# Optimization experiments

Measured on AMD Instinct MI355X. Metric: run time of the kernel, lower is better.

The kernel has to match this reference:

```python
import jax, jax.numpy as jnp
import numpy as np
from jax.ops import segment_sum

N_NODES = 100000
N_EDGES = 3200000
N_GRAPHS = 64


def gcn_conv(x, W, b, src, dst, n_nodes):
    # Linear transform first (PyG GCNConv applies lin before propagate)
    h = x @ W  # [N, out]
    # Add self loops
    loop = jnp.arange(n_nodes, dtype=src.dtype)
    s = jnp.concatenate([src, loop])
    d = jnp.concatenate([dst, loop])
    # Symmetric normalization deg^-1/2 (deg counts incoming edges incl. self loop)
    deg = segment_sum(jnp.ones_like(d, dtype=h.dtype), d, num_segments=n_nodes)
    dinv = jnp.where(deg > 0, jax.lax.rsqrt(deg), 0.0)
    norm = dinv[s] * dinv[d]  # [E+N]
    # Gather messages from source, scale, scatter-add to target
    msg = h[s] * norm[:, None]
    out = segment_sum(msg, d, num_segments=n_nodes)
    return out + b


def setup_inputs() -> dict:
    key = jax.random.key(0)
    ks = jax.random.split(key, 6)
    x = jax.random.normal(ks[0], (N_NODES, 128), dtype=jnp.float32)
    edge_index = jax.random.randint(ks[1], (2, N_EDGES), 0, N_NODES, dtype=jnp.int64)
    batch = jnp.sort(jax.random.randint(ks[2], (N_NODES,), 0, N_GRAPHS, dtype=jnp.int64))
    W1 = jax.random.normal(ks[3], (128, 256), dtype=jnp.float32) * (1.0 / np.sqrt(128))
    b1 = jnp.zeros((256,), dtype=jnp.float32)
    W2 = jax.random.normal(ks[4], (256, 128), dtype=jnp.float32) * (1.0 / np.sqrt(256))
    b2 = jnp.zeros((128,), dtype=jnp.float32)
    return {"x": x, "edge_index": edge_index, "batch": batch,
            "W1": W1, "b1": b1, "W2": W2, "b2": b2, "num_graphs": N_GRAPHS}


def reference(x, edge_index, batch, W1, b1, W2, b2, num_graphs):
    n_nodes = x.shape[0]
    src, dst = edge_index[0], edge_index[1]
    # dropout(p=0.6, training=False) is identity at inference
    h = jax.nn.relu(gcn_conv(x, W1, b1, src, dst, n_nodes))
    h = gcn_conv(h, W2, b2, src, dst, n_nodes)
    # global_mean_pool by graph id
    sums = segment_sum(h, batch, num_segments=num_graphs)
    counts = segment_sum(jnp.ones((n_nodes,), dtype=h.dtype), batch, num_segments=num_graphs)
    return sums / jnp.maximum(counts, 1.0)[:, None]
```

## Files before the change

### kernel.cpp

```cpp
#include <hip/hip_runtime.h>
#include <hip/hip_bf16.h>
#include <stdint.h>

#define N_NODES 100000
#define N_EDGES 3200000
#define N_GRAPHS 64
#define BSH 8
#define NB 391
#define G_SC 512
#define EPB 6250

typedef unsigned int u32;
typedef unsigned short u16;
typedef __attribute__((ext_vector_type(8))) short bf16x8;
typedef __attribute__((ext_vector_type(4))) float f32x4;

__device__ __forceinline__ float bf_lo(u32 u){ return __uint_as_float(u << 16); }
__device__ __forceinline__ float bf_hi(u32 u){ return __uint_as_float(u & 0xffff0000u); }
__device__ __forceinline__ u16 f2bf(float f){
    union { __hip_bfloat16 h; u16 u; } c; c.h = __float2bfloat16(f); return c.u;
}
__device__ __forceinline__ u32 pack2(float a, float b){
    return (u32)f2bf(a) | ((u32)f2bf(b) << 16);
}

__global__ __launch_bounds__(512) void k_hist(const int* __restrict__ dst,
                                              int* __restrict__ hist){
    __shared__ int h[NB];
    int tid = threadIdx.x, g = blockIdx.x;
    for (int i = tid; i < NB; i += 512) h[i] = 0;
    __syncthreads();
    const int2* d2 = reinterpret_cast<const int2*>(dst + g * EPB);
    for (int i = tid; i < EPB / 2; i += 512){
        int2 d = d2[i];
        atomicAdd(&h[d.x >> BSH], 1);
        atomicAdd(&h[d.y >> BSH], 1);
    }
    __syncthreads();
    for (int i = tid; i < NB; i += 512) hist[i * G_SC + g] = h[i];
}

__global__ __launch_bounds__(512) void k_colscan(const int* __restrict__ hist,
                                                 int* __restrict__ cursors,
                                                 int* __restrict__ btot){
    __shared__ int sm[512];
    int b = blockIdx.x, tid = threadIdx.x;
    int v = hist[b * G_SC + tid];
    sm[tid] = v; __syncthreads();
    for (int off = 1; off < 512; off <<= 1){
        int t = (tid >= off) ? sm[tid - off] : 0;
        __syncthreads(); sm[tid] += t; __syncthreads();
    }
    cursors[b * G_SC + tid] = sm[tid] - v;
    if (tid == 511) btot[b] = sm[511];
}

__global__ __launch_bounds__(512) void k_bscan(const int* __restrict__ btot,
                                               int* __restrict__ bbase){
    __shared__ int sm[512];
    int tid = threadIdx.x;
    int v = (tid < NB) ? btot[tid] : 0;
    sm[tid] = v; __syncthreads();
    for (int off = 1; off < 512; off <<= 1){
        int t = (tid >= off) ? sm[tid - off] : 0;
        __syncthreads(); sm[tid] += t; __syncthreads();
    }
    if (tid < NB) bbase[tid] = sm[tid] - v;
    if (tid == 0) bbase[NB] = N_EDGES;
}

__global__ __launch_bounds__(512) void k_scatter(const int* __restrict__ src,
                                                 const int* __restrict__ dst,
                                                 const int* __restrict__ cursors,
                                                 const int* __restrict__ bbase,
                                                 u32* __restrict__ pairs){
    __shared__ int cur[NB];
    int g = blockIdx.x, tid = threadIdx.x;
    for (int i = tid; i < NB; i += 512) cur[i] = cursors[i * G_SC + g] + bbase[i];
    __syncthreads();
    const int2* s2 = reinterpret_cast<const int2*>(src + g * EPB);
    const int2* d2 = reinterpret_cast<const int2*>(dst + g * EPB);
    for (int i = tid; i < EPB / 2; i += 512){
        int2 s = s2[i]; int2 d = d2[i];
        int p0 = atomicAdd(&cur[d.x >> BSH], 1);
        pairs[p0] = (u32)s.x | ((u32)(d.x & 255) << 24);
        int p1 = atomicAdd(&cur[d.y >> BSH], 1);
        pairs[p1] = (u32)s.y | ((u32)(d.y & 255) << 24);
    }
}

__global__ __launch_bounds__(512) void k_fine(const u32* __restrict__ pairs,
                                              const int* __restrict__ bbase,
                                              int* __restrict__ offsets,
                                              float* __restrict__ dinv,
                                              int* __restrict__ csr_src){
    __shared__ int ldeg[256];
    __shared__ int ssc[256];
    __shared__ int lcur[256];
    int b = blockIdx.x, tid = threadIdx.x;
    int node0 = b << BSH;
    if (tid < 256) ldeg[tid] = 0;
    __syncthreads();
    int e0 = bbase[b], e1 = bbase[b + 1];
    for (int e = e0 + tid; e < e1; e += 512)
        atomicAdd(&ldeg[pairs[e] >> 24], 1);
    __syncthreads();
    int myDeg = (tid < 256) ? ldeg[tid] : 0;
    if (tid < 256) ssc[tid] = myDeg;
    __syncthreads();
    for (int off = 1; off < 256; off <<= 1){
        int t = 0;
        if (tid >= off && tid < 256) t = ssc[tid - off];
        __syncthreads();
        if (tid < 256) ssc[tid] += t;
        __syncthreads();
    }
    if (tid < 256){
        int excl = ssc[tid] - myDeg;
        int n = node0 + tid;
        if (n <= N_NODES) offsets[n] = e0 + excl;
        if (n < N_NODES)  dinv[n] = rsqrtf((float)myDeg + 1.0f);
        lcur[tid] = e0 + excl;
    }
    __syncthreads();
    for (int e = e0 + tid; e < e1; e += 512){
        u32 p = pairs[e];
        int pos = atomicAdd(&lcur[p >> 24], 1);
        csr_src[pos] = (int)(p & 0xFFFFFFu);
    }
}

__global__ void k_cvt_x(const float* __restrict__ x, const float* __restrict__ dinv,
                        u32* __restrict__ xb){
    int i = blockIdx.x * blockDim.x + threadIdx.x;
    if (i < N_NODES * 32){
        float w = dinv[i >> 5];
        float4 f = reinterpret_cast<const float4*>(x)[i];
        uint2 p = make_uint2(pack2(f.x * w, f.y * w), pack2(f.z * w, f.w * w));
        reinterpret_cast<uint2*>(xb)[i] = p;
    }
}

__global__ void k_cvt_w(const float* __restrict__ W1, const float* __restrict__ W2,
                        u16* __restrict__ w1t, u16* __restrict__ w2t){
    int i = blockIdx.x * blockDim.x + threadIdx.x;
    if (i < 128 * 256){
        int n = i / 128, k = i % 128;
        w1t[i] = f2bf(W1[k * 256 + n]);
    } else {
        int j = i - 128 * 256;
        int n = j / 256, k = j % 256;
        w2t[j] = f2bf(W2[k * 128 + n]);
    }
}

template<bool OUT_BF16>
__global__ __launch_bounds__(256) void k_agg(const u32* __restrict__ X,
                      const int* __restrict__ offs, const int* __restrict__ csr_src,
                      const float* __restrict__ dinv, void* __restrict__ out){
    int lane = threadIdx.x & 63;
    int v = blockIdx.x * 4 + (threadIdx.x >> 6);
    u32 u = X[v * 64 + lane];
    float a0 = bf_lo(u), a1 = bf_hi(u);
    int e1 = offs[v + 1];
    for (int e = offs[v]; e < e1; e += 64){
        int idx = e + lane;
        int sv = (idx < e1) ? csr_src[idx] : 0;
        int cnt = min(64, e1 - e);
        int j = 0;
        for (; j + 8 <= cnt; j += 8){
            int s0 = __shfl(sv, j),   s1 = __shfl(sv, j+1), s2 = __shfl(sv, j+2), s3 = __shfl(sv, j+3);
            int s4 = __shfl(sv, j+4), s5 = __shfl(sv, j+5), s6 = __shfl(sv, j+6), s7 = __shfl(sv, j+7);
            u32 u0 = X[s0*64 + lane], u1 = X[s1*64 + lane], u2 = X[s2*64 + lane], u3 = X[s3*64 + lane];
            u32 u4 = X[s4*64 + lane], u5 = X[s5*64 + lane], u6 = X[s6*64 + lane], u7 = X[s7*64 + lane];
            a0 += (bf_lo(u0) + bf_lo(u1)) + (bf_lo(u2) + bf_lo(u3))
                + (bf_lo(u4) + bf_lo(u5)) + (bf_lo(u6) + bf_lo(u7));
            a1 += (bf_hi(u0) + bf_hi(u1)) + (bf_hi(u2) + bf_hi(u3))
                + (bf_hi(u4) + bf_hi(u5)) + (bf_hi(u6) + bf_hi(u7));
        }
        for (; j < cnt; j++){
            int s = __shfl(sv, j);
            u32 uu = X[s*64 + lane];
            a0 += bf_lo(uu); a1 += bf_hi(uu);
        }
    }
    float w = dinv[v];
    a0 *= w; a1 *= w;
    if (OUT_BF16){
        ((u32*)out)[v*64 + lane] = pack2(a0, a1);
    } else {
        ((float2*)out)[v*64 + lane] = make_float2(a0, a1);
    }
}

template<int BK, int BN, bool RELU, bool BIAS, bool SCALE>
__global__ __launch_bounds__(256) void k_gemm(const u16* __restrict__ A, const u16* __restrict__ BT,
                        const float* __restrict__ bias, const float* __restrict__ rowscale,
                        u16* __restrict__ C, int M){
    __shared__ char As[64 * BK * 2];
    const int tid = threadIdx.x;
    const int rowbytes = BK * 2;
    const int units = 8 * BK;
    for (int it = tid; it < units; it += 256){
        int flat = it * 16;
        int r = flat / rowbytes, cb = flat % rowbytes;
        int grow = blockIdx.x * 64 + r;
        int4 val = make_int4(0,0,0,0);
        if (grow < M) val = *reinterpret_cast<const int4*>(A + (size_t)grow * BK + cb / 2);
        *reinterpret_cast<int4*>(As + r * rowbytes + (cb ^ ((r & 7) << 4))) = val;
    }
    __syncthreads();

    const int wid = tid >> 6, lane = tid & 63;
    const int r0 = wid * 16;
    constexpr int NF = BN / 16;
    f32x4 acc[NF];
#pragma unroll
    for (int i = 0; i < NF; i++) acc[i] = (f32x4){0.f,0.f,0.f,0.f};
    const int ar = r0 + (lane & 15);
    const int koff = (lane >> 4) * 8;
#pragma unroll
    for (int kb = 0; kb < BK / 32; kb++){
        int kbyte = (kb * 32 + koff) * 2;
        bf16x8 aF = *reinterpret_cast<const bf16x8*>(As + ar * rowbytes + (kbyte ^ ((ar & 7) << 4)));
#pragma unroll
        for (int nf = 0; nf < NF; nf++){
            int bn = nf * 16 + (lane & 15);
            bf16x8 bF = *reinterpret_cast<const bf16x8*>(BT + bn * BK + kb * 32 + koff);
            acc[nf] = __builtin_amdgcn_mfma_f32_16x16x32_bf16(aF, bF, acc[nf], 0, 0, 0);
        }
    }
#pragma unroll
    for (int nf = 0; nf < NF; nf++){
        int col = nf * 16 + (lane & 15);
        float bv = BIAS ? bias[col] : 0.f;
#pragma unroll
        for (int j = 0; j < 4; j++){
            int grow = blockIdx.x * 64 + r0 + (lane >> 4) * 4 + j;
            if (grow < M){
                float val = acc[nf][j] + bv;
                if (RELU) val = fmaxf(val, 0.f);
                if (SCALE) val *= rowscale[grow];
                C[(size_t)grow * BN + col] = f2bf(val);
            }
        }
    }
}

__global__ void k_pool(const float* __restrict__ agg2f, const int* __restrict__ batch,
                       float* __restrict__ psum, float* __restrict__ counts){
    const int NPB = 100;
    int n0 = blockIdx.x * NPB, n1 = min(n0 + NPB, N_NODES);
    int tid = threadIdx.x;
    float racc = 0.f; int gcur = batch[n0]; int runlen = 0;
    for (int n = n0; n < n1; n++){
        int g = batch[n];
        if (g != gcur){
            atomicAdd(&psum[gcur * 128 + tid], racc);
            if (tid == 0) atomicAdd(&counts[gcur], (float)runlen);
            racc = 0.f; runlen = 0; gcur = g;
        }
        racc += agg2f[(size_t)n * 128 + tid];
        runlen++;
    }
    atomicAdd(&psum[gcur * 128 + tid], racc);
    if (tid == 0) atomicAdd(&counts[gcur], (float)runlen);
}

__global__ void k_final(const float* __restrict__ psum, const float* __restrict__ counts,
                        const float* __restrict__ b2, float* __restrict__ out){
    int g = blockIdx.x, c = threadIdx.x;
    out[g * 128 + c] = psum[g * 128 + c] / fmaxf(counts[g], 1.0f) + b2[c];
}

extern "C" void kernel_launch(void* const* d_in, const int* in_sizes, int n_in,
                              void* d_out, int out_size, void* d_ws, size_t ws_size,
                              hipStream_t stream){
    const float* x   = (const float*)d_in[0];
    const int*   ei  = (const int*)d_in[1];
    const int* batch = (const int*)d_in[2];
    const float* W1  = (const float*)d_in[3];
    const float* b1  = (const float*)d_in[4];
    const float* W2  = (const float*)d_in[5];
    const float* b2  = (const float*)d_in[6];
    float* out = (float*)d_out;
    const int* esrc = ei;
    const int* edst = ei + N_EDGES;

    char* w = (char*)d_ws;
    size_t off = 0;
    auto alloc = [&](size_t bytes) -> char* {
        char* p = w + off; off += (bytes + 255) & ~size_t(255); return p;
    };
    float* dinv     = (float*)alloc((size_t)N_NODES * 4);
    int*   offsets  = (int*)  alloc((size_t)(N_NODES + 1) * 4);
    int*   hist     = (int*)  alloc((size_t)NB * G_SC * 4);
    int*   cursors  = (int*)  alloc((size_t)NB * G_SC * 4);
    int*   btot     = (int*)  alloc((size_t)NB * 4);
    int*   bbase    = (int*)  alloc((size_t)(NB + 1) * 4);
    int*   csr_src  = (int*)  alloc((size_t)N_EDGES * 4);
    u32*   xb       = (u32*)  alloc((size_t)N_NODES * 64 * 4);
    u16*   aggx     = (u16*)  alloc((size_t)N_NODES * 128 * 2);
    u16*   h        = (u16*)  alloc((size_t)N_NODES * 256 * 2);
    u16*   t        = (u16*)  alloc((size_t)N_NODES * 128 * 2);
    u16*   w1t      = (u16*)  alloc(128 * 256 * 2);
    u16*   w2t      = (u16*)  alloc(256 * 128 * 2);
    float* psum     = (float*)alloc((size_t)N_GRAPHS * 128 * 4);
    float* counts   = (float*)alloc((size_t)N_GRAPHS * 4);
    float* agg2f    = (float*)h;
    u32*   pairs    = (u32*)h;

    hipMemsetAsync(psum, 0, (size_t)N_GRAPHS * 128 * 4, stream);
    hipMemsetAsync(counts, 0, (size_t)N_GRAPHS * 4, stream);

    k_hist   <<<G_SC, 512, 0, stream>>>(edst, hist);
    k_colscan<<<NB, 512, 0, stream>>>(hist, cursors, btot);
    k_bscan  <<<1, 512, 0, stream>>>(btot, bbase);
    k_scatter<<<G_SC, 512, 0, stream>>>(esrc, edst, cursors, bbase, pairs);
    k_fine   <<<NB, 512, 0, stream>>>(pairs, bbase, offsets, dinv, csr_src);

    k_cvt_x<<<12500, 256, 0, stream>>>(x, dinv, xb);
    k_cvt_w<<<256, 256, 0, stream>>>(W1, W2, w1t, w2t);

    k_agg<true><<<25000, 256, 0, stream>>>(xb, offsets, csr_src, dinv, aggx);
    k_gemm<128, 256, true, true, false><<<1563, 256, 0, stream>>>(
        aggx, w1t, b1, nullptr, h, N_NODES);
    k_gemm<256, 128, false, false, true><<<1563, 256, 0, stream>>>(
        h, w2t, nullptr, dinv, t, N_NODES);
    k_agg<false><<<25000, 256, 0, stream>>>((const u32*)t, offsets, csr_src, dinv, (void*)agg2f);
    k_pool <<<1000, 128, 0, stream>>>(agg2f, batch, psum, counts);
    k_final<<<N_GRAPHS, 128, 0, stream>>>(psum, counts, b2, out);
}
```

Measured before the change: 596.0 us.

## Halve coarse sort bucket size and store second aggregation output in bf16

The coarse destination buckets shrink from 256 to 128 nodes, doubling the bucket count (782). This gives more blocks for the column scan and fine-sort kernels, and the single-block bucket scan grows to 1024 threads. The second aggregation now writes bf16 instead of fp32, and the pooling kernel reads packed bf16 pairs with 64 threads, roughly halving that intermediate's traffic. Rounding the final per-node features to bf16 before mean pooling adds some precision loss, and the larger histogram/cursor arrays add scan work.

```diff
diff --git a/kernel.cpp b/kernel.cpp
--- a/kernel.cpp
+++ b/kernel.cpp
@@ -5,8 +5,9 @@
 #define N_NODES 100000
 #define N_EDGES 3200000
 #define N_GRAPHS 64
-#define BSH 8
-#define NB 391
+#define BSH 7
+#define NBK 128
+#define NB 782
 #define G_SC 512
 #define EPB 6250
 
@@ -55,13 +56,13 @@
     if (tid == 511) btot[b] = sm[511];
 }
 
-__global__ __launch_bounds__(512) void k_bscan(const int* __restrict__ btot,
-                                               int* __restrict__ bbase){
-    __shared__ int sm[512];
+__global__ __launch_bounds__(1024) void k_bscan(const int* __restrict__ btot,
+                                                int* __restrict__ bbase){
+    __shared__ int sm[1024];
     int tid = threadIdx.x;
     int v = (tid < NB) ? btot[tid] : 0;
     sm[tid] = v; __syncthreads();
-    for (int off = 1; off < 512; off <<= 1){
+    for (int off = 1; off < 1024; off <<= 1){
         int t = (tid >= off) ? sm[tid - off] : 0;
         __syncthreads(); sm[tid] += t; __syncthreads();
     }
@@ -83,9 +84,9 @@
     for (int i = tid; i < EPB / 2; i += 512){
         int2 s = s2[i]; int2 d = d2[i];
         int p0 = atomicAdd(&cur[d.x >> BSH], 1);
-        pairs[p0] = (u32)s.x | ((u32)(d.x & 255) << 24);
+        pairs[p0] = (u32)s.x | ((u32)(d.x & (NBK - 1)) << 24);
         int p1 = atomicAdd(&cur[d.y >> BSH], 1);
-        pairs[p1] = (u32)s.y | ((u32)(d.y & 255) << 24);
+        pairs[p1] = (u32)s.y | ((u32)(d.y & (NBK - 1)) << 24);
     }
 }
 
@@ -94,28 +95,28 @@
                                               int* __restrict__ offsets,
                                               float* __restrict__ dinv,
                                               int* __restrict__ csr_src){
-    __shared__ int ldeg[256];
-    __shared__ int ssc[256];
-    __shared__ int lcur[256];
+    __shared__ int ldeg[NBK];
+    __shared__ int ssc[NBK];
+    __shared__ int lcur[NBK];
     int b = blockIdx.x, tid = threadIdx.x;
     int node0 = b << BSH;
-    if (tid < 256) ldeg[tid] = 0;
+    if (tid < NBK) ldeg[tid] = 0;
     __syncthreads();
     int e0 = bbase[b], e1 = bbase[b + 1];
     for (int e = e0 + tid; e < e1; e += 512)
         atomicAdd(&ldeg[pairs[e] >> 24], 1);
     __syncthreads();
-    int myDeg = (tid < 256) ? ldeg[tid] : 0;
-    if (tid < 256) ssc[tid] = myDeg;
-    __syncthreads();
-    for (int off = 1; off < 256; off <<= 1){
+    int myDeg = (tid < NBK) ? ldeg[tid] : 0;
+    if (tid < NBK) ssc[tid] = myDeg;
+    __syncthreads();
+    for (int off = 1; off < NBK; off <<= 1){
         int t = 0;
-        if (tid >= off && tid < 256) t = ssc[tid - off];
+        if (tid >= off && tid < NBK) t = ssc[tid - off];
         __syncthreads();
-        if (tid < 256) ssc[tid] += t;
+        if (tid < NBK) ssc[tid] += t;
         __syncthreads();
     }
-    if (tid < 256){
+    if (tid < NBK){
         int excl = ssc[tid] - myDeg;
         int n = node0 + tid;
         if (n <= N_NODES) offsets[n] = e0 + excl;
@@ -154,10 +155,9 @@
     }
 }
 
-template<bool OUT_BF16>
 __global__ __launch_bounds__(256) void k_agg(const u32* __restrict__ X,
                       const int* __restrict__ offs, const int* __restrict__ csr_src,
-                      const float* __restrict__ dinv, void* __restrict__ out){
+                      const float* __restrict__ dinv, u32* __restrict__ out){
     int lane = threadIdx.x & 63;
     int v = blockIdx.x * 4 + (threadIdx.x >> 6);
     u32 u = X[v * 64 + lane];
@@ -185,12 +185,7 @@
         }
     }
     float w = dinv[v];
-    a0 *= w; a1 *= w;
-    if (OUT_BF16){
-        ((u32*)out)[v*64 + lane] = pack2(a0, a1);
-    } else {
-        ((float2*)out)[v*64 + lane] = make_float2(a0, a1);
-    }
+    out[v*64 + lane] = pack2(a0 * w, a1 * w);
 }
 
 template<int BK, int BN, bool RELU, bool BIAS, bool SCALE>
@@ -247,23 +242,26 @@
     }
 }
 
-__global__ void k_pool(const float* __restrict__ agg2f, const int* __restrict__ batch,
+__global__ void k_pool(const u32* __restrict__ t2, const int* __restrict__ batch,
                        float* __restrict__ psum, float* __restrict__ counts){
     const int NPB = 100;
     int n0 = blockIdx.x * NPB, n1 = min(n0 + NPB, N_NODES);
     int tid = threadIdx.x;
-    float racc = 0.f; int gcur = batch[n0]; int runlen = 0;
+    float r0 = 0.f, r1 = 0.f; int gcur = batch[n0]; int runlen = 0;
     for (int n = n0; n < n1; n++){
         int g = batch[n];
         if (g != gcur){
-            atomicAdd(&psum[gcur * 128 + tid], racc);
+            atomicAdd(&psum[gcur * 128 + 2 * tid], r0);
+            atomicAdd(&psum[gcur * 128 + 2 * tid + 1], r1);
             if (tid == 0) atomicAdd(&counts[gcur], (float)runlen);
-            racc = 0.f; runlen = 0; gcur = g;
-        }
-        racc += agg2f[(size_t)n * 128 + tid];
+            r0 = 0.f; r1 = 0.f; runlen = 0; gcur = g;
+        }
+        u32 u = t2[(size_t)n * 64 + tid];
+        r0 += bf_lo(u); r1 += bf_hi(u);
         runlen++;
     }
-    atomicAdd(&psum[gcur * 128 + tid], racc);
+    atomicAdd(&psum[gcur * 128 + 2 * tid], r0);
+    atomicAdd(&psum[gcur * 128 + 2 * tid + 1], r1);
     if (tid == 0) atomicAdd(&counts[gcur], (float)runlen);
 }
 
@@ -307,7 +305,7 @@
     u16*   w2t      = (u16*)  alloc(256 * 128 * 2);
     float* psum     = (float*)alloc((size_t)N_GRAPHS * 128 * 4);
     float* counts   = (float*)alloc((size_t)N_GRAPHS * 4);
-    float* agg2f    = (float*)h;
+    u32*   t2       = (u32*)h;
     u32*   pairs    = (u32*)h;
 
     hipMemsetAsync(psum, 0, (size_t)N_GRAPHS * 128 * 4, stream);
@@ -315,19 +313,19 @@
 
     k_hist   <<<G_SC, 512, 0, stream>>>(edst, hist);
     k_colscan<<<NB, 512, 0, stream>>>(hist, cursors, btot);
-    k_bscan  <<<1, 512, 0, stream>>>(btot, bbase);
+    k_bscan  <<<1, 1024, 0, stream>>>(btot, bbase);
     k_scatter<<<G_SC, 512, 0, stream>>>(esrc, edst, cursors, bbase, pairs);
     k_fine   <<<NB, 512, 0, stream>>>(pairs, bbase, offsets, dinv, csr_src);
 
     k_cvt_x<<<12500, 256, 0, stream>>>(x, dinv, xb);
     k_cvt_w<<<256, 256, 0, stream>>>(W1, W2, w1t, w2t);
 
-    k_agg<true><<<25000, 256, 0, stream>>>(xb, offsets, csr_src, dinv, aggx);
+    k_agg<<<25000, 256, 0, stream>>>(xb, offsets, csr_src, dinv, (u32*)aggx);
     k_gemm<128, 256, true, true, false><<<1563, 256, 0, stream>>>(
         aggx, w1t, b1, nullptr, h, N_NODES);
     k_gemm<256, 128, false, false, true><<<1563, 256, 0, stream>>>(
         h, w2t, nullptr, dinv, t, N_NODES);
-    k_agg<false><<<25000, 256, 0, stream>>>((const u32*)t, offsets, csr_src, dinv, (void*)agg2f);
-    k_pool <<<1000, 128, 0, stream>>>(agg2f, batch, psum, counts);
+    k_agg<<<25000, 256, 0, stream>>>((const u32*)t, offsets, csr_src, dinv, t2);
+    k_pool <<<1000, 64, 0, stream>>>(t2, batch, psum, counts);
     k_final<<<N_GRAPHS, 128, 0, stream>>>(psum, counts, b2, out);
 }
```

Result: slower. 610.8 us (+2.5%).
